# Optimization experiments

Hardware: AMD Instinct MI355X
Metric: run time of the kernel (lower is better)

The kernel has to match this reference:

```python
import jax, jax.numpy as jnp
import numpy as np

D = 768      # embedding_dim
H = 12       # num_heads
HS = D // H  # head_size = 64
B, T, TC = 8, 1024, 256
FF = 4 * D
EPS = 1e-5


def _layernorm(x, w, b):
    mu = jnp.mean(x, axis=-1, keepdims=True)
    var = jnp.mean((x - mu) ** 2, axis=-1, keepdims=True)
    return (x - mu) / jnp.sqrt(var + EPS) * w + b


def _mha(x_q, x_kv, Wq, bq, Wk, bk, Wv, bv):
    # Batched equivalent of the per-head Python loop: weights stacked as [H, D, HS].
    q = jnp.einsum('btd,hde->bhte', x_q, Wq) + bq[None, :, None, :]
    k = jnp.einsum('bsd,hde->bhse', x_kv, Wk) + bk[None, :, None, :]
    v = jnp.einsum('bsd,hde->bhse', x_kv, Wv) + bv[None, :, None, :]
    scale = HS ** (-0.5)  # original scales by C**-0.5 with C = head_size
    wei = jax.nn.softmax(jnp.einsum('bhte,bhse->bhts', q, k) * scale, axis=-1)
    o = jnp.einsum('bhts,bhse->bhte', wei, v)  # [B,H,T,HS]
    # torch.cat over heads on dim=-1 == transpose then merge head dims
    return o.transpose(0, 2, 1, 3).reshape(o.shape[0], o.shape[2], H * HS)


def setup_inputs() -> dict:
    key = jax.random.key(0)
    ks = jax.random.split(key, 20)
    s = 0.02
    inp = {
        'img_embedding': jax.random.normal(ks[0], (B, T, D), jnp.float32),
        'context': jax.random.normal(ks[1], (B, TC, D), jnp.float32),
        'ln1_w': jnp.ones((D,), jnp.float32), 'ln1_b': jnp.zeros((D,), jnp.float32),
        'sWq': jax.random.normal(ks[2], (H, D, HS), jnp.float32) * s,
        'sbq': jnp.zeros((H, HS), jnp.float32),
        'sWk': jax.random.normal(ks[3], (H, D, HS), jnp.float32) * s,
        'sbk': jnp.zeros((H, HS), jnp.float32),
        'sWv': jax.random.normal(ks[4], (H, D, HS), jnp.float32) * s,
        'sbv': jnp.zeros((H, HS), jnp.float32),
        'ln2_w': jnp.ones((D,), jnp.float32), 'ln2_b': jnp.zeros((D,), jnp.float32),
        'cWq': jax.random.normal(ks[5], (H, D, HS), jnp.float32) * s,
        'cbq': jnp.zeros((H, HS), jnp.float32),
        'cWk': jax.random.normal(ks[6], (H, D, HS), jnp.float32) * s,
        'cbk': jnp.zeros((H, HS), jnp.float32),
        'cWv': jax.random.normal(ks[7], (H, D, HS), jnp.float32) * s,
        'cbv': jnp.zeros((H, HS), jnp.float32),
        'ln3_w': jnp.ones((D,), jnp.float32), 'ln3_b': jnp.zeros((D,), jnp.float32),
        'W1': jax.random.normal(ks[8], (D, FF), jnp.float32) * s,
        'b1': jnp.zeros((FF,), jnp.float32),
        'W2': jax.random.normal(ks[9], (FF, D), jnp.float32) * s,
        'b2': jnp.zeros((D,), jnp.float32),
    }
    return inp


def reference(img_embedding, context, ln1_w, ln1_b, sWq, sbq, sWk, sbk, sWv, sbv,
              ln2_w, ln2_b, cWq, cbq, cWk, cbk, cWv, cbv, ln3_w, ln3_b,
              W1, b1, W2, b2):
    x = img_embedding
    x = x + _mha(_layernorm(x, ln1_w, ln1_b), _layernorm(x, ln1_w, ln1_b),
                 sWq, sbq, sWk, sbk, sWv, sbv)
    x = x + _mha(_layernorm(x, ln2_w, ln2_b), context,
                 cWq, cbq, cWk, cbk, cWv, cbv)
    h = _layernorm(x, ln3_w, ln3_b)
    ff = jax.nn.silu(h @ W1 + b1) @ W2 + b2
    return x + ff
```

## Files before the change

kernel.cpp:

```cpp
#include <hip/hip_runtime.h>
#include <hip/hip_bf16.h>


#define D_EMB 768
#define N_HEADS 12
#define HEAD 64
#define B_SZ 8
#define T_IMG 1024
#define T_CTX 256
#define FF_DIM 3072
#define ROWS_IMG (B_SZ * T_IMG)
#define ROWS_CTX (B_SZ * T_CTX)
#define BIGCOL (1 << 28)
#define PART_STRIDE (ROWS_IMG * D_EMB)

typedef __bf16 bf16x8 __attribute__((ext_vector_type(8)));
typedef __bf16 bf16x4 __attribute__((ext_vector_type(4)));
typedef float f32x4 __attribute__((ext_vector_type(4)));

__device__ __forceinline__ void gld16(const void* g, void* l) {
    __builtin_amdgcn_global_load_lds(
        (const __attribute__((address_space(1))) unsigned int*)g,
        (__attribute__((address_space(3))) unsigned int*)l, 16, 0, 0);
}

__global__ __launch_bounds__(256) void copy4_kernel(const float4* __restrict__ src,
                                                    float4* __restrict__ dst) {
    int i = blockIdx.x * 256 + threadIdx.x;
    dst[i] = src[i];
}

__global__ __launch_bounds__(256) void cvt_bf16_kernel(const float* __restrict__ src,
                                                       __bf16* __restrict__ dst, int n4) {
    int i = blockIdx.x * 256 + threadIdx.x;
    if (i >= n4) return;
    float4 v = ((const float4*)src)[i];
    __bf16* d = dst + i * 4;
    d[0] = (__bf16)v.x; d[1] = (__bf16)v.y; d[2] = (__bf16)v.z; d[3] = (__bf16)v.w;
}

__global__ __launch_bounds__(256) void reduce_w2_kernel(
    const __bf16* __restrict__ P, const float* __restrict__ b2,
    float* __restrict__ X) {
    int i = blockIdx.x * 256 + threadIdx.x;
    int base = i * 4;
    int col = base % D_EMB;
    bf16x4 p0 = *(const bf16x4*)&P[base];
    bf16x4 p1 = *(const bf16x4*)&P[PART_STRIDE + base];
    float4 x = *(float4*)&X[base];
    float4 bb = *(const float4*)&b2[col];
    x.x += (float)p0[0] + (float)p1[0] + bb.x;
    x.y += (float)p0[1] + (float)p1[1] + bb.y;
    x.z += (float)p0[2] + (float)p1[2] + bb.z;
    x.w += (float)p0[3] + (float)p1[3] + bb.w;
    *(float4*)&X[base] = x;
}

__global__ __launch_bounds__(256) void transpose_cvt_kernel(
    const float* __restrict__ src, __bf16* __restrict__ dst,
    int src_rows, int src_cols) {
    __shared__ float tile[64][65];
    int tid = threadIdx.x;
    int r0 = blockIdx.y * 64, c0 = blockIdx.x * 64;
    int lr = tid >> 4, lc = (tid & 15) * 4;
#pragma unroll
    for (int i = 0; i < 4; i++) {
        float4 v = *(const float4*)&src[(size_t)(r0 + i * 16 + lr) * src_cols + c0 + lc];
        tile[i * 16 + lr][lc] = v.x; tile[i * 16 + lr][lc + 1] = v.y;
        tile[i * 16 + lr][lc + 2] = v.z; tile[i * 16 + lr][lc + 3] = v.w;
    }
    __syncthreads();
#pragma unroll
    for (int i = 0; i < 4; i++) {
        int cc = i * 16 + lr;
        int rr = (tid & 15) * 4;
        bf16x4 o;
#pragma unroll
        for (int j = 0; j < 4; j++) o[j] = (__bf16)tile[rr + j][cc];
        *(bf16x4*)&dst[(size_t)(c0 + cc) * src_rows + r0 + rr] = o;
    }
}

__global__ __launch_bounds__(256) void repack_qkv_t_kernel(
    const float* __restrict__ Wq, const float* __restrict__ Wk, const float* __restrict__ Wv,
    const float* __restrict__ bq, const float* __restrict__ bk, const float* __restrict__ bv,
    __bf16* __restrict__ Wt, float* __restrict__ bp) {
    __shared__ float tile[64][65];
    int tid = threadIdx.x;
    int which = blockIdx.y / 12, h = blockIdx.y - which * 12;
    int d0 = blockIdx.x * 64;
    const float* W = (which == 0) ? Wq : ((which == 1) ? Wk : Wv);
    const float* src = W + ((size_t)h * D_EMB + d0) * HEAD;
    int lr = tid >> 4, lc = (tid & 15) * 4;
#pragma unroll
    for (int i = 0; i < 4; i++) {
        float4 v = *(const float4*)&src[(size_t)(i * 16 + lr) * HEAD + lc];
        tile[i * 16 + lr][lc] = v.x; tile[i * 16 + lr][lc + 1] = v.y;
        tile[i * 16 + lr][lc + 2] = v.z; tile[i * 16 + lr][lc + 3] = v.w;
    }
    __syncthreads();
#pragma unroll
    for (int i = 0; i < 4; i++) {
        int e = i * 16 + lr;
        int dd = (tid & 15) * 4;
        bf16x4 o;
#pragma unroll
        for (int j = 0; j < 4; j++) o[j] = (__bf16)tile[dd + j][e];
        *(bf16x4*)&Wt[(size_t)(which * 768 + h * 64 + e) * D_EMB + d0 + dd] = o;
    }
    if (blockIdx.x == 0 && tid < 64) {
        const float* bb = (which == 0) ? bq : ((which == 1) ? bk : bv);
        bp[which * 768 + h * 64 + tid] = bb[h * 64 + tid];
    }
}

__global__ __launch_bounds__(256) void ln_kernel(const float* __restrict__ x,
                                                 const float* __restrict__ lw,
                                                 const float* __restrict__ lb,
                                                 __bf16* __restrict__ y) {
    int row = blockIdx.x;
    int tid = threadIdx.x;
    const float* xr = x + (size_t)row * D_EMB;
    float a0 = xr[tid], a1 = xr[tid + 256], a2 = xr[tid + 512];
    float s = a0 + a1 + a2;
    float ss = a0 * a0 + a1 * a1 + a2 * a2;
#pragma unroll
    for (int off = 32; off > 0; off >>= 1) {
        s += __shfl_down(s, off, 64);
        ss += __shfl_down(ss, off, 64);
    }
    __shared__ float red[8];
    __shared__ float stats[2];
    int wv = tid >> 6, lane = tid & 63;
    if (lane == 0) { red[wv] = s; red[4 + wv] = ss; }
    __syncthreads();
    if (tid == 0) {
        float S = red[0] + red[1] + red[2] + red[3];
        float SS = red[4] + red[5] + red[6] + red[7];
        float mu = S * (1.0f / D_EMB);
        float var = SS * (1.0f / D_EMB) - mu * mu;
        stats[0] = mu;
        stats[1] = rsqrtf(var + 1e-5f);
    }
    __syncthreads();
    float mu = stats[0], rs = stats[1];
    __bf16* yr = y + (size_t)row * D_EMB;
    yr[tid]       = (__bf16)((a0 - mu) * rs * lw[tid]       + lb[tid]);
    yr[tid + 256] = (__bf16)((a1 - mu) * rs * lw[tid + 256] + lb[tid + 256]);
    yr[tid + 512] = (__bf16)((a2 - mu) * rs * lw[tid + 512] + lb[tid + 512]);
}

__global__ __launch_bounds__(256) void mfma_gemm_bt(
    const __bf16* __restrict__ A, int lda,
    const __bf16* __restrict__ Bt, int ldb,
    const float* __restrict__ bias,
    __bf16* __restrict__ Cb, int ldc,
    int Kc, int act, int qlimit,
    __bf16* __restrict__ VTout, int vtok, int vcol0, int kcol0, int kcol1) {
    __shared__ __bf16 As[128 * 32];
    __shared__ __bf16 Bs[128 * 32];
    int tid = threadIdx.x;
    int bx = blockIdx.x, by = blockIdx.y, kz = blockIdx.z;
    int w = tid >> 6, lane = tid & 63;
    int c = lane & 15, quad = lane >> 4;
    int wm = (w >> 1) * 64, wn = (w & 1) * 64;

    f32x4 acc[4][4];
#pragma unroll
    for (int i = 0; i < 4; i++)
#pragma unroll
        for (int j = 0; j < 4; j++) acc[i][j] = (f32x4){0.f, 0.f, 0.f, 0.f};

    int srow = tid >> 2;
    int scol = (tid & 3) * 8;
    const __bf16* Ag = A + (size_t)(by * 128 + srow) * lda + (size_t)kz * Kc + scol;
    const __bf16* Bg = Bt + (size_t)(bx * 128 + srow) * ldb + (size_t)kz * Kc + scol;
    char* AsB = (char*)As + w * 1024;
    char* BsB = (char*)Bs + w * 1024;

    for (int k0 = 0; k0 < Kc; k0 += 32) {
        gld16(Ag + k0, AsB);
        gld16(Ag + (size_t)64 * lda + k0, AsB + 4096);
        gld16(Bg + k0, BsB);
        gld16(Bg + (size_t)64 * ldb + k0, BsB + 4096);
        __syncthreads();
        bf16x8 af[4], bfr[4];
#pragma unroll
        for (int mi = 0; mi < 4; mi++)
            af[mi] = *(const bf16x8*)&As[(wm + mi * 16 + c) * 32 + quad * 8];
#pragma unroll
        for (int ni = 0; ni < 4; ni++)
            bfr[ni] = *(const bf16x8*)&Bs[(wn + ni * 16 + c) * 32 + quad * 8];
#pragma unroll
        for (int mi = 0; mi < 4; mi++)
#pragma unroll
            for (int ni = 0; ni < 4; ni++)
                acc[mi][ni] = __builtin_amdgcn_mfma_f32_16x16x32_bf16(
                    bfr[ni], af[mi], acc[mi][ni], 0, 0, 0);
        __syncthreads();
    }

#pragma unroll
    for (int mi = 0; mi < 4; mi++) {
#pragma unroll
        for (int ni = 0; ni < 4; ni++) {
            int row = by * 128 + wm + mi * 16 + c;
            int colbase = bx * 128 + wn + ni * 16 + quad * 4;
            float bvv[4] = {0.f, 0.f, 0.f, 0.f};
            if (bias && kz == 0) {
                float4 b4 = *(const float4*)&bias[colbase];
                bvv[0] = b4.x; bvv[1] = b4.y; bvv[2] = b4.z; bvv[3] = b4.w;
            }
            float qs = (colbase < qlimit) ? 0.125f : 1.0f;
            float v[4];
#pragma unroll
            for (int r = 0; r < 4; r++) {
                float t = (acc[mi][ni][r] + bvv[r]) * qs;
                if (act == 1) t = t / (1.0f + __expf(-t));
                v[r] = t;
            }
            if (VTout && colbase >= vcol0) {
                int hc = colbase - vcol0;
                int hh = hc >> 6, ebase = hc & 63;
                int tok = row;
#pragma unroll
                for (int r = 0; r < 4; r++) {
                    int e = ebase + r;
                    int sl = ((((tok >> 3) & 7) ^ (e & 7)) << 3) | (tok & 7);
                    VTout[(size_t)(hh * 64 + e) * vtok + (tok & ~63) + sl] = (__bf16)v[r];
                }
            } else if (colbase >= kcol0 && colbase < kcol1) {
                int hc = colbase - kcol0;
                int hh = hc >> 6, ebase = hc & 63;
                int tok = row;
                int es = (((ebase >> 3) ^ (tok & 7)) << 3) | (ebase & 7);
                bf16x4 pv;
#pragma unroll
                for (int r = 0; r < 4; r++) pv[r] = (__bf16)v[r];
                *(bf16x4*)&Cb[(size_t)tok * ldc + kcol0 + hh * 64 + es] = pv;
            } else {
                __bf16* dst = Cb + (size_t)kz * PART_STRIDE;
                bf16x4 pv;
#pragma unroll
                for (int r = 0; r < 4; r++) pv[r] = (__bf16)v[r];
                *(bf16x4*)&dst[(size_t)row * ldc + colbase] = pv;
            }
        }
    }
}

__device__ __forceinline__ void stage_half(const __bf16* __restrict__ G, int ld,
                                           int kcol, __bf16* lds_half, int tid) {
    int w = tid >> 6;
#pragma unroll
    for (int j = 0; j < 2; j++) {
        int oe = (j * 512 + tid) * 8;
        int r = oe >> 6;
        int colx = (oe & 63) ^ ((r & 7) << 3);
        gld16(G + (size_t)r * ld + kcol + colx,
              (char*)lds_half + (j * 512 + w * 64) * 16);
    }
}

__device__ __forceinline__ bf16x8 lds_frag(const __bf16* h, int row, int kk, int quad) {
    int off = (kk * 32 + quad * 8) ^ ((row & 7) << 3);
    return *(const bf16x8*)&h[row * 64 + off];
}

__global__ __launch_bounds__(512, 2) void mfma_gemm_bt256(
    const __bf16* __restrict__ A, int lda,
    const __bf16* __restrict__ Bt, int ldb,
    const float* __restrict__ bias,
    __bf16* __restrict__ Cb, int ldc,
    int Kc, int act, int qlimit,
    __bf16* __restrict__ VTout, int vtok, int vcol0, int kcol0, int kcol1) {
    __shared__ __bf16 SM[8 * 8192];
    int tid = threadIdx.x;
    int kz = blockIdx.z;
    int gx = gridDim.x;
    int nwg = gx * gridDim.y;
    int orig = blockIdx.y * gx + blockIdx.x;
    int swz = (orig & 7) * (nwg >> 3) + (orig >> 3);
    int bx = swz % gx, by = swz / gx;

    int w = tid >> 6, lane = tid & 63, c = lane & 15, quad = lane >> 4;
    int wr = w >> 2, wc = w & 3;
    int rBbase = (wc & 1) * 64;

    const __bf16* Ag0 = A + (size_t)(by * 256) * lda + (size_t)kz * Kc;
    const __bf16* Ag1 = Ag0 + (size_t)128 * lda;
    const __bf16* Bg0 = Bt + (size_t)(bx * 256) * ldb + (size_t)kz * Kc;
    const __bf16* Bg1 = Bg0 + (size_t)128 * ldb;

    f32x4 acc[8][4];
#pragma unroll
    for (int i = 0; i < 8; i++)
#pragma unroll
        for (int j = 0; j < 4; j++) acc[i][j] = (f32x4){0.f, 0.f, 0.f, 0.f};

    stage_half(Ag0, lda, 0, SM + 0 * 8192, tid);
    stage_half(Ag1, lda, 0, SM + 1 * 8192, tid);
    stage_half(Bg0, ldb, 0, SM + 2 * 8192, tid);
    stage_half(Bg1, ldb, 0, SM + 3 * 8192, tid);
    stage_half(Ag0, lda, 64, SM + 4 * 8192, tid);
    stage_half(Ag1, lda, 64, SM + 5 * 8192, tid);
    stage_half(Bg0, ldb, 64, SM + 6 * 8192, tid);
    stage_half(Bg1, ldb, 64, SM + 7 * 8192, tid);
    asm volatile("s_waitcnt vmcnt(8)" ::: "memory");
    __builtin_amdgcn_s_barrier();

    int nt = Kc >> 6;
    for (int t = 0; t < nt; t++) {
        int cur = (t & 1) << 2;
        const __bf16* Ah = SM + (cur + wr) * 8192;
        const __bf16* Bh = SM + (cur + 2 + (wc >> 1)) * 8192;
#pragma unroll
        for (int kk = 0; kk < 2; kk++) {
            bf16x8 bfr[4];
#pragma unroll
            for (int ni = 0; ni < 4; ni++)
                bfr[ni] = lds_frag(Bh, rBbase + ni * 16 + c, kk, quad);
#pragma unroll
            for (int mg = 0; mg < 2; mg++) {
                bf16x8 af[4];
#pragma unroll
                for (int mi = 0; mi < 4; mi++)
                    af[mi] = lds_frag(Ah, mg * 64 + mi * 16 + c, kk, quad);
                __builtin_amdgcn_s_setprio(1);
#pragma unroll
                for (int mi = 0; mi < 4; mi++)
#pragma unroll
                    for (int ni = 0; ni < 4; ni++)
                        acc[mg * 4 + mi][ni] = __builtin_amdgcn_mfma_f32_16x16x32_bf16(
                            bfr[ni], af[mi], acc[mg * 4 + mi][ni], 0, 0, 0);
                __builtin_amdgcn_s_setprio(0);
            }
        }
        if (t + 1 < nt) {
            __builtin_amdgcn_s_barrier();
            if (t + 2 < nt) {
                int kc = (t + 2) << 6;
                stage_half(Ag0, lda, kc, SM + (cur + 0) * 8192, tid);
                stage_half(Ag1, lda, kc, SM + (cur + 1) * 8192, tid);
                stage_half(Bg0, ldb, kc, SM + (cur + 2) * 8192, tid);
                stage_half(Bg1, ldb, kc, SM + (cur + 3) * 8192, tid);
                asm volatile("s_waitcnt vmcnt(8)" ::: "memory");
            } else {
                asm volatile("s_waitcnt vmcnt(0)" ::: "memory");
            }
            __builtin_amdgcn_s_barrier();
        }
    }

#pragma unroll
    for (int mi = 0; mi < 8; mi++) {
        int row = by * 256 + wr * 128 + (mi >> 2) * 64 + (mi & 3) * 16 + c;
#pragma unroll
        for (int ni = 0; ni < 4; ni++) {
            int colbase = bx * 256 + wc * 64 + ni * 16 + quad * 4;
            float bvv[4] = {0.f, 0.f, 0.f, 0.f};
            if (bias && kz == 0) {
                float4 b4 = *(const float4*)&bias[colbase];
                bvv[0] = b4.x; bvv[1] = b4.y; bvv[2] = b4.z; bvv[3] = b4.w;
            }
            float qs = (colbase < qlimit) ? 0.125f : 1.0f;
            float v[4];
#pragma unroll
            for (int r = 0; r < 4; r++) {
                float tv = (acc[mi][ni][r] + bvv[r]) * qs;
                if (act == 1) tv = tv / (1.0f + __expf(-tv));
                v[r] = tv;
            }
            if (VTout && colbase >= vcol0) {
                int hc = colbase - vcol0;
                int hh = hc >> 6, ebase = hc & 63;
                int tok = row;
#pragma unroll
                for (int r = 0; r < 4; r++) {
                    int e = ebase + r;
                    int sl = ((((tok >> 3) & 7) ^ (e & 7)) << 3) | (tok & 7);
                    VTout[(size_t)(hh * 64 + e) * vtok + (tok & ~63) + sl] = (__bf16)v[r];
                }
            } else if (colbase >= kcol0 && colbase < kcol1) {
                int hc = colbase - kcol0;
                int hh = hc >> 6, ebase = hc & 63;
                int tok = row;
                int es = (((ebase >> 3) ^ (tok & 7)) << 3) | (ebase & 7);
                bf16x4 pv;
#pragma unroll
                for (int r = 0; r < 4; r++) pv[r] = (__bf16)v[r];
                *(bf16x4*)&Cb[(size_t)tok * ldc + kcol0 + hh * 64 + es] = pv;
            } else {
                __bf16* dst = Cb + (size_t)kz * PART_STRIDE;
                bf16x4 pv;
#pragma unroll
                for (int r = 0; r < 4; r++) pv[r] = (__bf16)v[r];
                *(bf16x4*)&dst[(size_t)row * ldc + colbase] = pv;
            }
        }
    }
}

__global__ __launch_bounds__(128, 2) void mfma_attn(
    const __bf16* __restrict__ Q, int qld,
    const __bf16* __restrict__ Kp, int kld,
    const __bf16* __restrict__ VTg, int vtok,
    int kv_tokens, float* __restrict__ X) {
    __shared__ __bf16 Kt[64 * 64];
    __shared__ __bf16 VT[80 * 64];
    __shared__ __bf16 Ps[128 * 76];
    int tid = threadIdx.x;
    int qt = blockIdx.x & 7;
    int bh = blockIdx.x >> 3;
    int b = bh / N_HEADS, h = bh - b * N_HEADS;
    int w = tid >> 6, lane = tid & 63, c = lane & 15, quad = lane >> 4;
    int q0 = qt * 128;

    for (int i = tid; i < 16 * 64; i += 128)
        VT[64 * 64 + i] = (i < 64) ? (__bf16)1.0f : (__bf16)0.0f;

    {
        const __bf16* Qg = Q + (size_t)(b * T_IMG + q0 + (tid >> 3)) * qld
                           + h * HEAD + (tid & 7) * 8;
        char* QsB = (char*)Ps + w * 1024;
#pragma unroll
        for (int j = 0; j < 8; j++)
            gld16(Qg + (size_t)j * 16 * qld, QsB + j * 2048);
    }
    __syncthreads();
    bf16x8 qa[4][2];
#pragma unroll
    for (int st = 0; st < 4; st++)
#pragma unroll
        for (int ch = 0; ch < 2; ch++)
            qa[st][ch] = *(const bf16x8*)&Ps[(w * 64 + st * 16 + c) * 64 + ch * 32 + quad * 8];
    __syncthreads();

    f32x4 o[4][5];
#pragma unroll
    for (int st = 0; st < 4; st++)
#pragma unroll
        for (int ut = 0; ut < 5; ut++) o[st][ut] = (f32x4){0.f, 0.f, 0.f, 0.f};

    char* KtB = (char*)Kt + w * 1024;
    char* VtB = (char*)VT + w * 1024;
    int ntiles = kv_tokens >> 6;
    for (int t = 0; t < ntiles; t++) {
        const __bf16* Kg = Kp + (size_t)(b * kv_tokens + t * 64 + (tid >> 3)) * kld
                           + h * HEAD + (tid & 7) * 8;
        const __bf16* Vg = VTg + (size_t)(h * HEAD + (tid >> 3)) * vtok
                           + b * kv_tokens + t * 64 + (tid & 7) * 8;
#pragma unroll
        for (int j = 0; j < 4; j++) {
            gld16(Kg + (size_t)j * 16 * kld, KtB + j * 2048);
            gld16(Vg + (size_t)j * 16 * vtok, VtB + j * 2048);
        }
        __syncthreads();

        bf16x8 kb[4][2];
#pragma unroll
        for (int nt = 0; nt < 4; nt++)
#pragma unroll
            for (int ch = 0; ch < 2; ch++)
                kb[nt][ch] = *(const bf16x8*)&Kt[(nt * 16 + c) * 64
                                + (((ch * 4 + quad) ^ (c & 7)) << 3)];
#pragma unroll
        for (int st = 0; st < 4; st++) {
            f32x4 s[4];
#pragma unroll
            for (int nt = 0; nt < 4; nt++) {
                s[nt] = (f32x4){0.f, 0.f, 0.f, 0.f};
                s[nt] = __builtin_amdgcn_mfma_f32_16x16x32_bf16(kb[nt][0], qa[st][0], s[nt], 0, 0, 0);
                s[nt] = __builtin_amdgcn_mfma_f32_16x16x32_bf16(kb[nt][1], qa[st][1], s[nt], 0, 0, 0);
            }
#pragma unroll
            for (int nt = 0; nt < 4; nt++) {
                bf16x4 pk;
#pragma unroll
                for (int r = 0; r < 4; r++) pk[r] = (__bf16)__expf(s[nt][r]);
                *(bf16x4*)&Ps[(size_t)(w * 64 + st * 16 + c) * 76 + nt * 16 + quad * 4] = pk;
            }
        }
        __syncthreads();

        bf16x8 vb[5][2];
#pragma unroll
        for (int ut = 0; ut < 5; ut++)
#pragma unroll
            for (int ch = 0; ch < 2; ch++)
                vb[ut][ch] = *(const bf16x8*)&VT[(ut * 16 + c) * 64
                                + (((ch * 4 + quad) ^ (c & 7)) << 3)];
#pragma unroll
        for (int st = 0; st < 4; st++) {
            bf16x8 pa0 = *(const bf16x8*)&Ps[(w * 64 + st * 16 + c) * 76 + quad * 8];
            bf16x8 pa1 = *(const bf16x8*)&Ps[(w * 64 + st * 16 + c) * 76 + 32 + quad * 8];
#pragma unroll
            for (int ut = 0; ut < 5; ut++) {
                o[st][ut] = __builtin_amdgcn_mfma_f32_16x16x32_bf16(pa0, vb[ut][0], o[st][ut], 0, 0, 0);
                o[st][ut] = __builtin_amdgcn_mfma_f32_16x16x32_bf16(pa1, vb[ut][1], o[st][ut], 0, 0, 0);
            }
        }
        __syncthreads();
    }

#pragma unroll
    for (int st = 0; st < 4; st++) {
        float lr[4];
#pragma unroll
        for (int r = 0; r < 4; r++) lr[r] = __shfl(o[st][4][r], lane & 48, 64);
#pragma unroll
        for (int ut = 0; ut < 4; ut++) {
#pragma unroll
            for (int r = 0; r < 4; r++) {
                int row = b * T_IMG + q0 + w * 64 + st * 16 + quad * 4 + r;
                int col = h * HEAD + ut * 16 + c;
                X[(size_t)row * D_EMB + col] += o[st][ut][r] / lr[r];
            }
        }
    }
}

extern "C" void kernel_launch(void* const* d_in, const int* in_sizes, int n_in,
                              void* d_out, int out_size, void* d_ws, size_t ws_size,
                              hipStream_t stream) {
    const float* img  = (const float*)d_in[0];
    const float* ctx  = (const float*)d_in[1];
    const float* ln1w = (const float*)d_in[2];  const float* ln1b = (const float*)d_in[3];
    const float* sWq  = (const float*)d_in[4];  const float* sbq  = (const float*)d_in[5];
    const float* sWk  = (const float*)d_in[6];  const float* sbk  = (const float*)d_in[7];
    const float* sWv  = (const float*)d_in[8];  const float* sbv  = (const float*)d_in[9];
    const float* ln2w = (const float*)d_in[10]; const float* ln2b = (const float*)d_in[11];
    const float* cWq  = (const float*)d_in[12]; const float* cbq  = (const float*)d_in[13];
    const float* cWk  = (const float*)d_in[14]; const float* cbk  = (const float*)d_in[15];
    const float* cWv  = (const float*)d_in[16]; const float* cbv  = (const float*)d_in[17];
    const float* ln3w = (const float*)d_in[18]; const float* ln3b = (const float*)d_in[19];
    const float* W1   = (const float*)d_in[20]; const float* b1   = (const float*)d_in[21];
    const float* W2   = (const float*)d_in[22]; const float* b2   = (const float*)d_in[23];

    float* X = (float*)d_out;

    char* p = (char*)d_ws;
    __bf16* LNb  = (__bf16*)p; p += (size_t)ROWS_IMG * D_EMB * 2;
    __bf16* VTg  = (__bf16*)p; p += (size_t)12 * 64 * ROWS_IMG * 2;
    __bf16* BIG  = (__bf16*)p; p += (size_t)ROWS_IMG * FF_DIM * 2;
    __bf16* ctxb = (__bf16*)p; p += (size_t)ROWS_CTX * D_EMB * 2;
    __bf16* Wt   = (__bf16*)p; p += (size_t)2304 * 768 * 2;
    __bf16* cWt  = (__bf16*)p; p += (size_t)2304 * 768 * 2;
    __bf16* W1t  = (__bf16*)p; p += (size_t)FF_DIM * 768 * 2;
    __bf16* W2t  = (__bf16*)p; p += (size_t)768 * FF_DIM * 2;
    __bf16* VTc  = (__bf16*)p; p += (size_t)12 * 64 * ROWS_CTX * 2;
    float*  bp   = (float*)p;  p += 2304 * 4;
    float*  cbp  = (float*)p;  p += 2304 * 4;
    __bf16* Pk   = LNb;
    __bf16* QKVb = BIG;
    __bf16* Qc   = BIG;
    __bf16* KVc  = BIG + (size_t)ROWS_IMG * 768;
    __bf16* FFh  = BIG;

    copy4_kernel<<<ROWS_IMG * D_EMB / 4 / 256, 256, 0, stream>>>(
        (const float4*)img, (float4*)X);
    cvt_bf16_kernel<<<(ROWS_CTX * D_EMB / 4 + 255) / 256, 256, 0, stream>>>(
        ctx, ctxb, ROWS_CTX * D_EMB / 4);
    repack_qkv_t_kernel<<<dim3(12, 36), 256, 0, stream>>>(
        sWq, sWk, sWv, sbq, sbk, sbv, Wt, bp);
    repack_qkv_t_kernel<<<dim3(12, 36), 256, 0, stream>>>(
        cWq, cWk, cWv, cbq, cbk, cbv, cWt, cbp);
    transpose_cvt_kernel<<<dim3(FF_DIM / 64, 768 / 64), 256, 0, stream>>>(
        W1, W1t, 768, FF_DIM);
    transpose_cvt_kernel<<<dim3(768 / 64, FF_DIM / 64), 256, 0, stream>>>(
        W2, W2t, FF_DIM, 768);

    ln_kernel<<<ROWS_IMG, 256, 0, stream>>>(X, ln1w, ln1b, LNb);
    mfma_gemm_bt256<<<dim3(2304 / 256, ROWS_IMG / 256), 512, 0, stream>>>(
        LNb, D_EMB, Wt, D_EMB, bp, QKVb, 2304, D_EMB, 0, 768,
        VTg, ROWS_IMG, 1536, 768, 1536);
    mfma_attn<<<96 * 8, 128, 0, stream>>>(
        QKVb, 2304, QKVb + 768, 2304, VTg, ROWS_IMG, T_IMG, X);

    ln_kernel<<<ROWS_IMG, 256, 0, stream>>>(X, ln2w, ln2b, LNb);
    mfma_gemm_bt<<<dim3(768 / 128, ROWS_IMG / 128), 256, 0, stream>>>(
        LNb, D_EMB, cWt, D_EMB, cbp, Qc, 768, D_EMB, 0, 768,
        nullptr, 0, BIGCOL, BIGCOL, BIGCOL);
    mfma_gemm_bt<<<dim3(1536 / 128, ROWS_CTX / 128), 256, 0, stream>>>(
        ctxb, D_EMB, cWt + (size_t)768 * 768, D_EMB, cbp + 768,
        KVc, 1536, D_EMB, 0, 0,
        VTc, ROWS_CTX, 768, 0, 768);
    mfma_attn<<<96 * 8, 128, 0, stream>>>(
        Qc, 768, KVc, 1536, VTc, ROWS_CTX, T_CTX, X);

    ln_kernel<<<ROWS_IMG, 256, 0, stream>>>(X, ln3w, ln3b, LNb);
    mfma_gemm_bt256<<<dim3(FF_DIM / 256, ROWS_IMG / 256), 512, 0, stream>>>(
        LNb, D_EMB, W1t, D_EMB, b1, FFh, FF_DIM, D_EMB, 1, 0,
        nullptr, 0, BIGCOL, BIGCOL, BIGCOL);
    mfma_gemm_bt256<<<dim3(768 / 256, ROWS_IMG / 256, 2), 512, 0, stream>>>(
        FFh, FF_DIM, W2t, FF_DIM, nullptr, Pk, D_EMB, 1536, 0, 0,
        nullptr, 0, BIGCOL, BIGCOL, BIGCOL);
    reduce_w2_kernel<<<ROWS_IMG * D_EMB / 4 / 256, 256, 0, stream>>>(Pk, b2, X);
}
```

Before: 511.8 us.

## Fuse residual adds into attention and W2 GEMM, restructure 256-tile GEMM pipeline

```diff
diff --git a/kernel.cpp b/kernel.cpp
--- a/kernel.cpp
+++ b/kernel.cpp
@@ -12,7 +12,6 @@
 #define ROWS_IMG (B_SZ * T_IMG)
 #define ROWS_CTX (B_SZ * T_CTX)
 #define BIGCOL (1 << 28)
-#define PART_STRIDE (ROWS_IMG * D_EMB)
 
 typedef __bf16 bf16x8 __attribute__((ext_vector_type(8)));
 typedef __bf16 bf16x4 __attribute__((ext_vector_type(4)));
@@ -22,12 +21,6 @@
     __builtin_amdgcn_global_load_lds(
         (const __attribute__((address_space(1))) unsigned int*)g,
         (__attribute__((address_space(3))) unsigned int*)l, 16, 0, 0);
-}
-
-__global__ __launch_bounds__(256) void copy4_kernel(const float4* __restrict__ src,
-                                                    float4* __restrict__ dst) {
-    int i = blockIdx.x * 256 + threadIdx.x;
-    dst[i] = src[i];
 }
 
 __global__ __launch_bounds__(256) void cvt_bf16_kernel(const float* __restrict__ src,
@@ -37,23 +30,6 @@
     float4 v = ((const float4*)src)[i];
     __bf16* d = dst + i * 4;
     d[0] = (__bf16)v.x; d[1] = (__bf16)v.y; d[2] = (__bf16)v.z; d[3] = (__bf16)v.w;
-}
-
-__global__ __launch_bounds__(256) void reduce_w2_kernel(
-    const __bf16* __restrict__ P, const float* __restrict__ b2,
-    float* __restrict__ X) {
-    int i = blockIdx.x * 256 + threadIdx.x;
-    int base = i * 4;
-    int col = base % D_EMB;
-    bf16x4 p0 = *(const bf16x4*)&P[base];
-    bf16x4 p1 = *(const bf16x4*)&P[PART_STRIDE + base];
-    float4 x = *(float4*)&X[base];
-    float4 bb = *(const float4*)&b2[col];
-    x.x += (float)p0[0] + (float)p1[0] + bb.x;
-    x.y += (float)p0[1] + (float)p1[1] + bb.y;
-    x.z += (float)p0[2] + (float)p1[2] + bb.z;
-    x.w += (float)p0[3] + (float)p1[3] + bb.w;
-    *(float4*)&X[base] = x;
 }
 
 __global__ __launch_bounds__(256) void transpose_cvt_kernel(
@@ -156,11 +132,12 @@
     const float* __restrict__ bias,
     __bf16* __restrict__ Cb, int ldc,
     int Kc, int act, int qlimit,
-    __bf16* __restrict__ VTout, int vtok, int vcol0, int kcol0, int kcol1) {
+    __bf16* __restrict__ VTout, int vtok, int vcol0, int kcol0, int kcol1,
+    float* __restrict__ Xres) {
     __shared__ __bf16 As[128 * 32];
     __shared__ __bf16 Bs[128 * 32];
     int tid = threadIdx.x;
-    int bx = blockIdx.x, by = blockIdx.y, kz = blockIdx.z;
+    int bx = blockIdx.x, by = blockIdx.y;
     int w = tid >> 6, lane = tid & 63;
     int c = lane & 15, quad = lane >> 4;
     int wm = (w >> 1) * 64, wn = (w & 1) * 64;
@@ -173,8 +150,8 @@
 
     int srow = tid >> 2;
     int scol = (tid & 3) * 8;
-    const __bf16* Ag = A + (size_t)(by * 128 + srow) * lda + (size_t)kz * Kc + scol;
-    const __bf16* Bg = Bt + (size_t)(bx * 128 + srow) * ldb + (size_t)kz * Kc + scol;
+    const __bf16* Ag = A + (size_t)(by * 128 + srow) * lda + scol;
+    const __bf16* Bg = Bt + (size_t)(bx * 128 + srow) * ldb + scol;
     char* AsB = (char*)As + w * 1024;
     char* BsB = (char*)Bs + w * 1024;
 
@@ -207,7 +184,7 @@
             int row = by * 128 + wm + mi * 16 + c;
             int colbase = bx * 128 + wn + ni * 16 + quad * 4;
             float bvv[4] = {0.f, 0.f, 0.f, 0.f};
-            if (bias && kz == 0) {
+            if (bias) {
                 float4 b4 = *(const float4*)&bias[colbase];
                 bvv[0] = b4.x; bvv[1] = b4.y; bvv[2] = b4.z; bvv[3] = b4.w;
             }
@@ -219,7 +196,11 @@
                 if (act == 1) t = t / (1.0f + __expf(-t));
                 v[r] = t;
             }
-            if (VTout && colbase >= vcol0) {
+            if (Xres) {
+                float4 x4 = *(float4*)&Xres[(size_t)row * D_EMB + colbase];
+                x4.x += v[0]; x4.y += v[1]; x4.z += v[2]; x4.w += v[3];
+                *(float4*)&Xres[(size_t)row * D_EMB + colbase] = x4;
+            } else if (VTout && colbase >= vcol0) {
                 int hc = colbase - vcol0;
                 int hh = hc >> 6, ebase = hc & 63;
                 int tok = row;
@@ -239,26 +220,12 @@
                 for (int r = 0; r < 4; r++) pv[r] = (__bf16)v[r];
                 *(bf16x4*)&Cb[(size_t)tok * ldc + kcol0 + hh * 64 + es] = pv;
             } else {
-                __bf16* dst = Cb + (size_t)kz * PART_STRIDE;
                 bf16x4 pv;
 #pragma unroll
                 for (int r = 0; r < 4; r++) pv[r] = (__bf16)v[r];
-                *(bf16x4*)&dst[(size_t)row * ldc + colbase] = pv;
-            }
-        }
-    }
-}
-
-__device__ __forceinline__ void stage_half(const __bf16* __restrict__ G, int ld,
-                                           int kcol, __bf16* lds_half, int tid) {
-    int w = tid >> 6;
-#pragma unroll
-    for (int j = 0; j < 2; j++) {
-        int oe = (j * 512 + tid) * 8;
-        int r = oe >> 6;
-        int colx = (oe & 63) ^ ((r & 7) << 3);
-        gld16(G + (size_t)r * ld + kcol + colx,
-              (char*)lds_half + (j * 512 + w * 64) * 16);
+                *(bf16x4*)&Cb[(size_t)row * ldc + colbase] = pv;
+            }
+        }
     }
 }
 
@@ -267,16 +234,54 @@
     return *(const bf16x8*)&h[row * 64 + off];
 }
 
-__global__ __launch_bounds__(512, 2) void mfma_gemm_bt256(
-    const __bf16* __restrict__ A, int lda,
-    const __bf16* __restrict__ Bt, int ldb,
+template <int LDA_T, int LDB_T>
+__device__ __forceinline__ void stage256(const __bf16* a_, const __bf16* b_,
+                                         __bf16* da_) {
+    __bf16* db_ = da_ + 16384;
+#pragma unroll
+    for (int i = 0; i < 4; i++) {
+        gld16(a_ + (size_t)(i * 64) * LDA_T, da_ + i * 4096);
+        gld16(b_ + (size_t)(i * 64) * LDB_T, db_ + i * 4096);
+    }
+}
+
+__device__ __forceinline__ void compute256(const __bf16* base, int wr, int wc,
+                                           int c, int quad, int rBbase,
+                                           f32x4 (&acc)[8][4]) {
+    const __bf16* Ah = base + wr * 8192;
+    const __bf16* Bh = base + 16384 + (wc >> 1) * 8192;
+#pragma unroll
+    for (int kk = 0; kk < 2; kk++) {
+        bf16x8 bfr[4];
+#pragma unroll
+        for (int ni = 0; ni < 4; ni++)
+            bfr[ni] = lds_frag(Bh, rBbase + ni * 16 + c, kk, quad);
+#pragma unroll
+        for (int mg = 0; mg < 2; mg++) {
+            bf16x8 af[4];
+#pragma unroll
+            for (int mi = 0; mi < 4; mi++)
+                af[mi] = lds_frag(Ah, mg * 64 + mi * 16 + c, kk, quad);
+#pragma unroll
+            for (int mi = 0; mi < 4; mi++)
+#pragma unroll
+                for (int ni = 0; ni < 4; ni++)
+                    acc[mg * 4 + mi][ni] = __builtin_amdgcn_mfma_f32_16x16x32_bf16(
+                        bfr[ni], af[mi], acc[mg * 4 + mi][ni], 0, 0, 0);
+        }
+    }
+}
+
+template <int LDA_T, int LDB_T>
+__global__ __launch_bounds__(512, 2) void gemm256_2ph(
+    const __bf16* __restrict__ A,
+    const __bf16* __restrict__ Bt,
     const float* __restrict__ bias,
     __bf16* __restrict__ Cb, int ldc,
     int Kc, int act, int qlimit,
     __bf16* __restrict__ VTout, int vtok, int vcol0, int kcol0, int kcol1) {
-    __shared__ __bf16 SM[8 * 8192];
+    __shared__ __bf16 SM[2 * 4 * 8192];
     int tid = threadIdx.x;
-    int kz = blockIdx.z;
     int gx = gridDim.x;
     int nwg = gx * gridDim.y;
     int orig = blockIdx.y * gx + blockIdx.x;
@@ -287,10 +292,12 @@
     int wr = w >> 2, wc = w & 3;
     int rBbase = (wc & 1) * 64;
 
-    const __bf16* Ag0 = A + (size_t)(by * 256) * lda + (size_t)kz * Kc;
-    const __bf16* Ag1 = Ag0 + (size_t)128 * lda;
-    const __bf16* Bg0 = Bt + (size_t)(bx * 256) * ldb + (size_t)kz * Kc;
-    const __bf16* Bg1 = Bg0 + (size_t)128 * ldb;
+    int srow = tid >> 3;
+    int scol = ((tid & 7) * 8) ^ ((srow & 7) * 8);
+    const __bf16* Asrc = A + (size_t)(by * 256 + srow) * LDA_T + scol;
+    const __bf16* Bsrc = Bt + (size_t)(bx * 256 + srow) * LDB_T + scol;
+    __bf16* dst0 = SM + w * 512;
+    __bf16* dst1 = SM + 32768 + w * 512;
 
     f32x4 acc[8][4];
 #pragma unroll
@@ -298,57 +305,20 @@
 #pragma unroll
         for (int j = 0; j < 4; j++) acc[i][j] = (f32x4){0.f, 0.f, 0.f, 0.f};
 
-    stage_half(Ag0, lda, 0, SM + 0 * 8192, tid);
-    stage_half(Ag1, lda, 0, SM + 1 * 8192, tid);
-    stage_half(Bg0, ldb, 0, SM + 2 * 8192, tid);
-    stage_half(Bg1, ldb, 0, SM + 3 * 8192, tid);
-    stage_half(Ag0, lda, 64, SM + 4 * 8192, tid);
-    stage_half(Ag1, lda, 64, SM + 5 * 8192, tid);
-    stage_half(Bg0, ldb, 64, SM + 6 * 8192, tid);
-    stage_half(Bg1, ldb, 64, SM + 7 * 8192, tid);
-    asm volatile("s_waitcnt vmcnt(8)" ::: "memory");
-    __builtin_amdgcn_s_barrier();
+    stage256<LDA_T, LDB_T>(Asrc, Bsrc, dst0);
+    __syncthreads();
 
     int nt = Kc >> 6;
-    for (int t = 0; t < nt; t++) {
-        int cur = (t & 1) << 2;
-        const __bf16* Ah = SM + (cur + wr) * 8192;
-        const __bf16* Bh = SM + (cur + 2 + (wc >> 1)) * 8192;
-#pragma unroll
-        for (int kk = 0; kk < 2; kk++) {
-            bf16x8 bfr[4];
-#pragma unroll
-            for (int ni = 0; ni < 4; ni++)
-                bfr[ni] = lds_frag(Bh, rBbase + ni * 16 + c, kk, quad);
-#pragma unroll
-            for (int mg = 0; mg < 2; mg++) {
-                bf16x8 af[4];
-#pragma unroll
-                for (int mi = 0; mi < 4; mi++)
-                    af[mi] = lds_frag(Ah, mg * 64 + mi * 16 + c, kk, quad);
-                __builtin_amdgcn_s_setprio(1);
-#pragma unroll
-                for (int mi = 0; mi < 4; mi++)
-#pragma unroll
-                    for (int ni = 0; ni < 4; ni++)
-                        acc[mg * 4 + mi][ni] = __builtin_amdgcn_mfma_f32_16x16x32_bf16(
-                            bfr[ni], af[mi], acc[mg * 4 + mi][ni], 0, 0, 0);
-                __builtin_amdgcn_s_setprio(0);
-            }
-        }
+    for (int t = 0; t < nt; t += 2) {
+        if (t + 1 < nt)
+            stage256<LDA_T, LDB_T>(Asrc + (t + 1) * 64, Bsrc + (t + 1) * 64, dst1);
+        compute256(SM, wr, wc, c, quad, rBbase, acc);
+        __syncthreads();
         if (t + 1 < nt) {
-            __builtin_amdgcn_s_barrier();
-            if (t + 2 < nt) {
-                int kc = (t + 2) << 6;
-                stage_half(Ag0, lda, kc, SM + (cur + 0) * 8192, tid);
-                stage_half(Ag1, lda, kc, SM + (cur + 1) * 8192, tid);
-                stage_half(Bg0, ldb, kc, SM + (cur + 2) * 8192, tid);
-                stage_half(Bg1, ldb, kc, SM + (cur + 3) * 8192, tid);
-                asm volatile("s_waitcnt vmcnt(8)" ::: "memory");
-            } else {
-                asm volatile("s_waitcnt vmcnt(0)" ::: "memory");
-            }
-            __builtin_amdgcn_s_barrier();
+            if (t + 2 < nt)
+                stage256<LDA_T, LDB_T>(Asrc + (t + 2) * 64, Bsrc + (t + 2) * 64, dst0);
+            compute256(SM + 32768, wr, wc, c, quad, rBbase, acc);
+            __syncthreads();
         }
     }
 
@@ -359,7 +329,7 @@
         for (int ni = 0; ni < 4; ni++) {
             int colbase = bx * 256 + wc * 64 + ni * 16 + quad * 4;
             float bvv[4] = {0.f, 0.f, 0.f, 0.f};
-            if (bias && kz == 0) {
+            if (bias) {
                 float4 b4 = *(const float4*)&bias[colbase];
                 bvv[0] = b4.x; bvv[1] = b4.y; bvv[2] = b4.z; bvv[3] = b4.w;
             }
@@ -391,11 +361,10 @@
                 for (int r = 0; r < 4; r++) pv[r] = (__bf16)v[r];
                 *(bf16x4*)&Cb[(size_t)tok * ldc + kcol0 + hh * 64 + es] = pv;
             } else {
-                __bf16* dst = Cb + (size_t)kz * PART_STRIDE;
                 bf16x4 pv;
 #pragma unroll
                 for (int r = 0; r < 4; r++) pv[r] = (__bf16)v[r];
-                *(bf16x4*)&dst[(size_t)row * ldc + colbase] = pv;
+                *(bf16x4*)&Cb[(size_t)row * ldc + colbase] = pv;
             }
         }
     }
@@ -405,7 +374,7 @@
     const __bf16* __restrict__ Q, int qld,
     const __bf16* __restrict__ Kp, int kld,
     const __bf16* __restrict__ VTg, int vtok,
-    int kv_tokens, float* __restrict__ X) {
+    int kv_tokens, float* __restrict__ X, const float* __restrict__ Xin) {
     __shared__ __bf16 Kt[64 * 64];
     __shared__ __bf16 VT[80 * 64];
     __shared__ __bf16 Ps[128 * 76];
@@ -514,7 +483,9 @@
             for (int r = 0; r < 4; r++) {
                 int row = b * T_IMG + q0 + w * 64 + st * 16 + quad * 4 + r;
                 int col = h * HEAD + ut * 16 + c;
-                X[(size_t)row * D_EMB + col] += o[st][ut][r] / lr[r];
+                size_t idx = (size_t)row * D_EMB + col;
+                float base = Xin ? Xin[idx] : X[idx];
+                X[idx] = base + o[st][ut][r] / lr[r];
             }
         }
     }
@@ -551,14 +522,11 @@
     __bf16* VTc  = (__bf16*)p; p += (size_t)12 * 64 * ROWS_CTX * 2;
     float*  bp   = (float*)p;  p += 2304 * 4;
     float*  cbp  = (float*)p;  p += 2304 * 4;
-    __bf16* Pk   = LNb;
     __bf16* QKVb = BIG;
     __bf16* Qc   = BIG;
     __bf16* KVc  = BIG + (size_t)ROWS_IMG * 768;
     __bf16* FFh  = BIG;
 
-    copy4_kernel<<<ROWS_IMG * D_EMB / 4 / 256, 256, 0, stream>>>(
-        (const float4*)img, (float4*)X);
     cvt_bf16_kernel<<<(ROWS_CTX * D_EMB / 4 + 255) / 256, 256, 0, stream>>>(
         ctx, ctxb, ROWS_CTX * D_EMB / 4);
     repack_qkv_t_kernel<<<dim3(12, 36), 256, 0, stream>>>(
@@ -570,30 +538,29 @@
     transpose_cvt_kernel<<<dim3(768 / 64, FF_DIM / 64), 256, 0, stream>>>(
         W2, W2t, FF_DIM, 768);
 
-    ln_kernel<<<ROWS_IMG, 256, 0, stream>>>(X, ln1w, ln1b, LNb);
-    mfma_gemm_bt256<<<dim3(2304 / 256, ROWS_IMG / 256), 512, 0, stream>>>(
-        LNb, D_EMB, Wt, D_EMB, bp, QKVb, 2304, D_EMB, 0, 768,
+    ln_kernel<<<ROWS_IMG, 256, 0, stream>>>(img, ln1w, ln1b, LNb);
+    gemm256_2ph<768, 768><<<dim3(2304 / 256, ROWS_IMG / 256), 512, 0, stream>>>(
+        LNb, Wt, bp, QKVb, 2304, D_EMB, 0, 768,
         VTg, ROWS_IMG, 1536, 768, 1536);
     mfma_attn<<<96 * 8, 128, 0, stream>>>(
-        QKVb, 2304, QKVb + 768, 2304, VTg, ROWS_IMG, T_IMG, X);
+        QKVb, 2304, QKVb + 768, 2304, VTg, ROWS_IMG, T_IMG, X, img);
 
     ln_kernel<<<ROWS_IMG, 256, 0, stream>>>(X, ln2w, ln2b, LNb);
     mfma_gemm_bt<<<dim3(768 / 128, ROWS_IMG / 128), 256, 0, stream>>>(
         LNb, D_EMB, cWt, D_EMB, cbp, Qc, 768, D_EMB, 0, 768,
-        nullptr, 0, BIGCOL, BIGCOL, BIGCOL);
+        nullptr, 0, BIGCOL, BIGCOL, BIGCOL, nullptr);
     mfma_gemm_bt<<<dim3(1536 / 128, ROWS_CTX / 128), 256, 0, stream>>>(
         ctxb, D_EMB, cWt + (size_t)768 * 768, D_EMB, cbp + 768,
         KVc, 1536, D_EMB, 0, 0,
-        VTc, ROWS_CTX, 768, 0, 768);
+        VTc, ROWS_CTX, 768, 0, 768, nullptr);
     mfma_attn<<<96 * 8, 128, 0, stream>>>(
-        Qc, 768, KVc, 1536, VTc, ROWS_CTX, T_CTX, X);
+        Qc, 768, KVc, 1536, VTc, ROWS_CTX, T_CTX, X, nullptr);
 
     ln_kernel<<<ROWS_IMG, 256, 0, stream>>>(X, ln3w, ln3b, LNb);
-    mfma_gemm_bt256<<<dim3(FF_DIM / 256, ROWS_IMG / 256), 512, 0, stream>>>(
-        LNb, D_EMB, W1t, D_EMB, b1, FFh, FF_DIM, D_EMB, 1, 0,
+    gemm256_2ph<768, 768><<<dim3(FF_DIM / 256, ROWS_IMG / 256), 512, 0, stream>>>(
+        LNb, W1t, b1, FFh, FF_DIM, D_EMB, 1, 0,
         nullptr, 0, BIGCOL, BIGCOL, BIGCOL);
-    mfma_gemm_bt256<<<dim3(768 / 256, ROWS_IMG / 256, 2), 512, 0, stream>>>(
-        FFh, FF_DIM, W2t, FF_DIM, nullptr, Pk, D_EMB, 1536, 0, 0,
-        nullptr, 0, BIGCOL, BIGCOL, BIGCOL);
-    reduce_w2_kernel<<<ROWS_IMG * D_EMB / 4 / 256, 256, 0, stream>>>(Pk, b2, X);
-}
+    mfma_gemm_bt<<<dim3(768 / 128, ROWS_IMG / 128), 256, 0, stream>>>(
+        FFh, FF_DIM, W2t, FF_DIM, b2, nullptr, D_EMB, FF_DIM, 0, 0,
+        nullptr, 0, BIGCOL, BIGCOL, BIGCOL, X);
+}
```

After: 565.3 us. 1.1x slower.
